# Kernel tuning notes

Hardware: AMD Instinct MI355X
Metric: run time of the kernel (lower is better)

The kernel has to match this reference:

```python
import jax, jax.numpy as jnp
import numpy as np

N = 16384
E = 262144
IN = 512
H = 64
K = 8


def setup_inputs() -> dict:
    key = jax.random.key(0)
    ks = jax.random.split(key, 16)
    def lin(k, fan_in, fan_out):
        # xavier_uniform
        lim = float(np.sqrt(6.0 / (fan_in + fan_out)))
        return jax.random.uniform(k, (fan_in, fan_out), jnp.float32, -lim, lim)
    inp = {
        'x': jax.random.normal(ks[0], (N, IN), jnp.float32),
        'edge_index': jax.random.randint(ks[1], (2, E), 0, N, jnp.int64) if jax.config.read('jax_enable_x64') else jax.random.randint(ks[1], (2, E), 0, N, jnp.int32),
        'W1': lin(ks[2], IN, H), 'b1': jnp.zeros((H,), jnp.float32),
        'W2': lin(ks[3], H, H), 'b2': jnp.zeros((H,), jnp.float32),
        'W3': lin(ks[4], H, H), 'b3': jnp.zeros((H,), jnp.float32),
        'W4': lin(ks[5], H, H), 'b4': jnp.zeros((H,), jnp.float32),
        'Wg1': lin(ks[6], H, H), 'bg1': jnp.zeros((H,), jnp.float32),
        'Wg2': lin(ks[7], H, H), 'bg2': jnp.zeros((H,), jnp.float32),
    }
    return inp


def reference(x, edge_index, W1, b1, W2, b2, W3, b3, W4, b4, Wg1, bg1, Wg2, bg2):
    n = x.shape[0]
    row, col = edge_index[0], edge_index[1]
    # symmetric-normalized Laplacian action: L v = v - D^-1/2 A D^-1/2 v
    deg = jax.ops.segment_sum(jnp.ones(row.shape[0], x.dtype), row, num_segments=n)
    dinv = jnp.where(deg > 0, jax.lax.rsqrt(jnp.maximum(deg, 1e-30)), 0.0)
    # spectral embedding MLP stack (dropout=0 -> identity)
    h = jnp.maximum(x @ W1 + b1, 0.0) @ W2 + b2
    h = jnp.maximum(h @ W3 + b3, 0.0) @ W4 + b4
    g = jnp.maximum(h @ Wg1 + bg1, 0.0) @ Wg2 + bg2  # [N, H]
    msg = (dinv[row] * dinv[col])[:, None] * g[col]   # [E, H]
    agg = jax.ops.segment_sum(msg, row, num_segments=n)
    filtered = g - agg                                 # L @ gft_x
    sim = filtered @ filtered.T                        # [N, N], dominant cost
    topk_vals, topk_idx = jax.lax.top_k(sim, K)        # [N, K]
    src = jnp.repeat(jnp.arange(n, dtype=topk_idx.dtype), K)
    new_edge_index = jnp.stack([src, topk_idx.reshape(-1)])  # [2, N*K]
    return topk_vals, new_edge_index
```

## Files before the change

kernel.cpp:

```cpp
#include <hip/hip_runtime.h>
#include <hip/hip_bf16.h>

#define N_NODES 16384
#define E_EDGES 262144
#define IN_DIM 512
#define KKEEP 56

#define AGG_SCALE 1099511627776.0
#define AGG_INV   (1.0/1099511627776.0)

typedef __attribute__((ext_vector_type(8))) short bf16x8;
typedef __attribute__((ext_vector_type(4))) float f32x4;

__device__ __forceinline__ int detect64(const void* __restrict__ ei) {
    const unsigned long long v = ((const unsigned long long*)ei)[threadIdx.x & 63];
    return __all(v < 16384ull) ? 1 : 0;
}

__device__ __forceinline__ int edge_at(const void* __restrict__ ei, int is64, int pos) {
    return is64 ? (int)(((const long long*)ei)[pos]) : ((const int*)ei)[pos];
}

__global__ __launch_bounds__(256) void deg_kernel(const void* __restrict__ ei,
                                                  int* __restrict__ deg) {
    const int is64 = detect64(ei);
    int e = blockIdx.x * 256 + threadIdx.x;
    int r = edge_at(ei, is64, e);
    if (r >= 0 && r < N_NODES) atomicAdd(&deg[r], 1);
}

__global__ __launch_bounds__(256) void scan_kernel(const int* __restrict__ deg, int* __restrict__ offs,
                                                   float* __restrict__ dinv) {
    __shared__ int part[257];
    const int t = threadIdx.x;
    const int base = t * 64;
    int s = 0;
    #pragma unroll 4
    for (int i = 0; i < 64; ++i) s += deg[base + i];
    part[t + 1] = s;
    if (t == 0) part[0] = 0;
    __syncthreads();
    if (t == 0) {
        int acc = 0;
        for (int i = 1; i <= 256; ++i) { acc += part[i]; part[i] = acc; }
    }
    __syncthreads();
    int run = part[t];
    for (int i = 0; i < 64; ++i) {
        const int d = deg[base + i];
        offs[base + i] = run; run += d;
        dinv[base + i] = (d > 0) ? __fdiv_rn(1.0f, __fsqrt_rn((float)d)) : 0.0f;
    }
    if (t == 255) offs[N_NODES] = run;
}

__global__ __launch_bounds__(256) void scatter_kernel(
    const void* __restrict__ ei,
    const int* __restrict__ offs, int* __restrict__ cursor, int* __restrict__ ecol_s)
{
    const int is64 = detect64(ei);
    int e = blockIdx.x * 256 + threadIdx.x;
    int r  = edge_at(ei, is64, e);
    if (r < 0 || r >= N_NODES) return;
    int cc = edge_at(ei, is64, E_EDGES + e);
    int pos = atomicAdd(&cursor[r], 1);
    ecol_s[offs[r] + pos] = (cc >= 0 && cc < N_NODES) ? cc : -1;
}

__device__ __forceinline__ void dense_layer32(float (*hsw)[64], int c,
                                              const float* __restrict__ WP,
                                              const float* __restrict__ BP,
                                              bool relu, bool last,
                                              float* __restrict__ gout, int n0)
{
    float s0 = 0.0f, s1 = 0.0f, s2 = 0.0f, s3 = 0.0f;
    #pragma unroll 4
    for (int k = 0; k < 64; k += 4) {
        const float4 h0 = *(const float4*)&hsw[0][k];
        const float4 h1 = *(const float4*)&hsw[1][k];
        const float4 h2 = *(const float4*)&hsw[2][k];
        const float4 h3 = *(const float4*)&hsw[3][k];
        const float w0 = WP[k * 64 + c];
        const float w1 = WP[(k + 1) * 64 + c];
        const float w2 = WP[(k + 2) * 64 + c];
        const float w3 = WP[(k + 3) * 64 + c];
        s0 = fmaf(h0.x, w0, s0); s0 = fmaf(h0.y, w1, s0); s0 = fmaf(h0.z, w2, s0); s0 = fmaf(h0.w, w3, s0);
        s1 = fmaf(h1.x, w0, s1); s1 = fmaf(h1.y, w1, s1); s1 = fmaf(h1.z, w2, s1); s1 = fmaf(h1.w, w3, s1);
        s2 = fmaf(h2.x, w0, s2); s2 = fmaf(h2.y, w1, s2); s2 = fmaf(h2.z, w2, s2); s2 = fmaf(h2.w, w3, s2);
        s3 = fmaf(h3.x, w0, s3); s3 = fmaf(h3.y, w1, s3); s3 = fmaf(h3.z, w2, s3); s3 = fmaf(h3.w, w3, s3);
    }
    const float bv = BP[c];
    s0 += bv; s1 += bv; s2 += bv; s3 += bv;
    if (relu) { s0 = fmaxf(s0, 0.0f); s1 = fmaxf(s1, 0.0f); s2 = fmaxf(s2, 0.0f); s3 = fmaxf(s3, 0.0f); }
    __syncthreads();
    if (last) {
        gout[(size_t)(n0 + 0) * 64 + c] = s0;
        gout[(size_t)(n0 + 1) * 64 + c] = s1;
        gout[(size_t)(n0 + 2) * 64 + c] = s2;
        gout[(size_t)(n0 + 3) * 64 + c] = s3;
    } else {
        hsw[0][c] = s0; hsw[1][c] = s1; hsw[2][c] = s2; hsw[3][c] = s3;
    }
    __syncthreads();
}

__global__ __launch_bounds__(256) void mlp_kernel(
    const float* __restrict__ x,
    const float* __restrict__ W1, const float* __restrict__ b1,
    const float* __restrict__ W2, const float* __restrict__ b2,
    const float* __restrict__ W3, const float* __restrict__ b3,
    const float* __restrict__ W4, const float* __restrict__ b4,
    const float* __restrict__ Wg1, const float* __restrict__ bg1,
    const float* __restrict__ Wg2, const float* __restrict__ bg2,
    float* __restrict__ g32)
{
    __shared__ float hs[4][4][64];
    const int w = threadIdx.x >> 6;
    const int c = threadIdx.x & 63;
    const int n0 = blockIdx.x * 16 + w * 4;

    float a0 = 0.0f, a1 = 0.0f, a2 = 0.0f, a3 = 0.0f;
    const float* xp = x + (size_t)n0 * IN_DIM;
    #pragma unroll 2
    for (int k = 0; k < IN_DIM; k += 4) {
        const float4 x0 = *(const float4*)(xp + k);
        const float4 x1 = *(const float4*)(xp + IN_DIM + k);
        const float4 x2 = *(const float4*)(xp + 2 * IN_DIM + k);
        const float4 x3 = *(const float4*)(xp + 3 * IN_DIM + k);
        const float w0 = W1[k * 64 + c];
        const float w1 = W1[(k + 1) * 64 + c];
        const float w2 = W1[(k + 2) * 64 + c];
        const float w3 = W1[(k + 3) * 64 + c];
        a0 = fmaf(x0.x, w0, a0); a0 = fmaf(x0.y, w1, a0); a0 = fmaf(x0.z, w2, a0); a0 = fmaf(x0.w, w3, a0);
        a1 = fmaf(x1.x, w0, a1); a1 = fmaf(x1.y, w1, a1); a1 = fmaf(x1.z, w2, a1); a1 = fmaf(x1.w, w3, a1);
        a2 = fmaf(x2.x, w0, a2); a2 = fmaf(x2.y, w1, a2); a2 = fmaf(x2.z, w2, a2); a2 = fmaf(x2.w, w3, a2);
        a3 = fmaf(x3.x, w0, a3); a3 = fmaf(x3.y, w1, a3); a3 = fmaf(x3.z, w2, a3); a3 = fmaf(x3.w, w3, a3);
    }
    const float bv = b1[c];
    hs[w][0][c] = fmaxf(a0 + bv, 0.0f);
    hs[w][1][c] = fmaxf(a1 + bv, 0.0f);
    hs[w][2][c] = fmaxf(a2 + bv, 0.0f);
    hs[w][3][c] = fmaxf(a3 + bv, 0.0f);
    __syncthreads();

    dense_layer32(hs[w], c, W2, b2, false, false, g32, n0);
    dense_layer32(hs[w], c, W3, b3, true,  false, g32, n0);
    dense_layer32(hs[w], c, W4, b4, false, false, g32, n0);
    dense_layer32(hs[w], c, Wg1, bg1, true, false, g32, n0);
    dense_layer32(hs[w], c, Wg2, bg2, false, true, g32, n0);
}

__global__ __launch_bounds__(256) void aggcsr_kernel(
    const int* __restrict__ offs, const int* __restrict__ ecol_s,
    const float* __restrict__ dinv, const float* __restrict__ g32,
    float* __restrict__ F32, short* __restrict__ Fb)
{
    const int r = (blockIdx.x << 2) + (threadIdx.x >> 6);
    const int h = threadIdx.x & 63;
    const float dr = dinv[r];
    const int b = offs[r], e2 = offs[r + 1];
    long long sum = 0;
    #pragma unroll 8
    for (int i = b; i < e2; ++i) {
        const int cc = ecol_s[i];
        if (cc < 0) continue;
        const float m = __fmul_rn(__fmul_rn(dr, dinv[cc]), g32[((size_t)cc << 6) + h]);
        sum += __double2ll_rn((double)m * AGG_SCALE);
    }
    const float a = (float)((double)sum * AGG_INV);
    const int idx = (r << 6) + h;
    const float f = g32[idx] - a;
    F32[idx] = f;
    __hip_bfloat16 hb = __float2bfloat16(f);
    Fb[idx] = *(short*)&hb;
}

__device__ __forceinline__ void ins6(unsigned* k, unsigned x) {
    const unsigned r0 = max(k[0], x);
    k[5] = min(k[4], max(k[5], x));
    k[4] = min(k[3], max(k[4], x));
    k[3] = min(k[2], max(k[3], x));
    k[2] = min(k[1], max(k[2], x));
    k[1] = min(k[0], max(k[1], x));
    k[0] = r0;
}

__global__ __launch_bounds__(256) void screen_kernel(
    const short* __restrict__ Fb, unsigned* __restrict__ cand)
{
    __shared__ short Bt[2][128 * 64];
    const int l = threadIdx.x & 63;
    const int w = threadIdx.x >> 6;
    const int rb = blockIdx.x >> 1;
    const int sp = blockIdx.x & 1;
    const int r0 = rb * 64 + w * 16;
    const int c0 = sp * 8192;

    const short* ap = Fb + ((size_t)(r0 + (l & 15)) << 6) + ((l >> 4) << 3);
    const bf16x8 a0 = *(const bf16x8*)(ap);
    const bf16x8 a1 = *(const bf16x8*)(ap + 32);

    unsigned keys[4][6];
    #pragma unroll
    for (int r = 0; r < 4; ++r)
        #pragma unroll
        for (int t = 0; t < 6; ++t) keys[r][t] = 0u;

    const int scol = threadIdx.x & 127;
    const int jb = (threadIdx.x >> 7) * 4;
    const short* gsrc0 = Fb + ((size_t)(c0 + scol) << 6) + jb * 8;

    bf16x8 st[4];
    #pragma unroll
    for (int j = 0; j < 4; ++j) st[j] = *(const bf16x8*)(gsrc0 + j * 8);
    #pragma unroll
    for (int j = 0; j < 4; ++j)
        *(bf16x8*)(&Bt[0][scol * 64 + (((jb + j) ^ (scol & 7)) << 3)]) = st[j];
    #pragma unroll
    for (int j = 0; j < 4; ++j) st[j] = *(const bf16x8*)(gsrc0 + (1 << 13) + j * 8);
    __syncthreads();

    const unsigned invb = 0x80000000u | (unsigned)(16383 - c0 - (l & 15));
    const int g0 = (l >> 4) ^ (l & 7);
    const int g1 = ((l >> 4) + 4) ^ (l & 7);
    int cur = 0;

    #pragma unroll 1
    for (int t = 0; t < 64; ++t) {
        const short* B = &Bt[cur][0];
        bf16x8 bf[16];
        #pragma unroll
        for (int s = 0; s < 8; ++s) {
            const int C = s * 16 + (l & 15);
            bf[2 * s]     = *(const bf16x8*)(B + C * 64 + (g0 << 3));
            bf[2 * s + 1] = *(const bf16x8*)(B + C * 64 + (g1 << 3));
        }
        if (t + 1 < 64) {
            #pragma unroll
            for (int j = 0; j < 4; ++j)
                *(bf16x8*)(&Bt[cur ^ 1][scol * 64 + (((jb + j) ^ (scol & 7)) << 3)]) = st[j];
        }
        if (t + 2 < 64) {
            const short* gs = gsrc0 + ((size_t)(t + 2) << 13);
            #pragma unroll
            for (int j = 0; j < 4; ++j) st[j] = *(const bf16x8*)(gs + j * 8);
        }
        #pragma unroll
        for (int s = 0; s < 8; ++s) {
            f32x4 acc = {0.0f, 0.0f, 0.0f, 0.0f};
            acc = __builtin_amdgcn_mfma_f32_16x16x32_bf16(a0, bf[2 * s], acc, 0, 0, 0);
            acc = __builtin_amdgcn_mfma_f32_16x16x32_bf16(a1, bf[2 * s + 1], acc, 0, 0, 0);
            const unsigned xv = invb - (unsigned)((t << 7) + (s << 4));
            #pragma unroll
            for (int r = 0; r < 4; ++r) {
                const unsigned key = (__float_as_uint(acc[r]) & 0xFFFFC000u) ^ xv;
                ins6(keys[r], key);
            }
        }
        __syncthreads();
        cur ^= 1;
    }

    #pragma unroll
    for (int r = 0; r < 4; ++r) {
        const int row = r0 + ((l >> 4) << 2) + r;
        unsigned* cp = cand + ((size_t)(sp * N_NODES + row)) * 96 + (l & 15) * 6;
        #pragma unroll
        for (int t = 0; t < 6; ++t) cp[t] = keys[r][t];
    }
}

__global__ __launch_bounds__(512) void refine2_kernel(
    const float* __restrict__ F, const unsigned* __restrict__ cand,
    float* __restrict__ out)
{
    __shared__ unsigned skey[2][192];
    __shared__ int clist[2][64];
    __shared__ float scand[2][KKEEP * 68];
    const int tid = threadIdx.x;
    const int half = tid >> 8;
    const int th = tid & 255;

    const int ksp = (th >= 96) ? 1 : 0;
    const int kslot = th - 96 * ksp;

    unsigned kreg = 0u;
    {
        const int row0 = blockIdx.x * 2 + half;
        if (th < 192) kreg = cand[((size_t)(ksp * N_NODES + row0)) * 96 + kslot];
    }

    #pragma unroll 1
    for (int i = 0; i < 8; ++i) {
        const int row = blockIdx.x * 2 + half + i * 2048;
        if (th < 192) skey[half][th] = kreg;
        __syncthreads();

        if (i + 1 < 8 && th < 192)
            kreg = cand[((size_t)(ksp * N_NODES + (row + 2048))) * 96 + kslot];

        if (th < 64) {
            const unsigned k0 = skey[half][th], k1 = skey[half][th + 64], k2 = skey[half][th + 128];
            unsigned long long lo = 0, hi = 0xFFFFFFFFull;
            while (hi - lo > 1) {
                const unsigned mid = (unsigned)((lo + hi) >> 1);
                const int cnt = __popcll(__ballot(k0 >= mid)) +
                                __popcll(__ballot(k1 >= mid)) +
                                __popcll(__ballot(k2 >= mid));
                if (cnt >= KKEEP) lo = mid; else hi = mid;
            }
            const unsigned thr = (unsigned)lo;
            const unsigned long long m0 = __ballot(k0 >= thr);
            const unsigned long long m1 = __ballot(k1 >= thr);
            const unsigned long long m2 = __ballot(k2 >= thr);
            const unsigned long long ltm = (1ull << th) - 1ull;
            const int b1 = __popcll(m0), b2 = b1 + __popcll(m1);
            if (k0 >= thr) clist[half][__popcll(m0 & ltm)]      = 16383 - (int)(k0 & 0x3FFFu);
            if (k1 >= thr) clist[half][b1 + __popcll(m1 & ltm)] = 16383 - (int)(k1 & 0x3FFFu);
            if (k2 >= thr) clist[half][b2 + __popcll(m2 & ltm)] = 16383 - (int)(k2 & 0x3FFFu);
        }
        __syncthreads();

        if (th < KKEEP * 4) {
            const int g = th >> 2, sub = th & 3;
            const float* src = F + ((size_t)clist[half][g] << 6) + sub * 16;
            float* dst = &scand[half][g * 68 + sub * 16];
            #pragma unroll
            for (int j = 0; j < 4; ++j)
                *(float4*)(dst + 4 * j) = *(const float4*)(src + 4 * j);
        }
        __syncthreads();

        float val = -3.4e38f; int idx = 1 << 30;
        if (th < KKEEP) {
            idx = clist[half][th];
            const float* fp = &scand[half][th * 68];
            const float* frp = F + ((size_t)row << 6);
            float acc = 0.0f;
            #pragma unroll 4
            for (int j = 0; j < 16; ++j) {
                const float4 a = *(const float4*)(frp + 4 * j);
                const float4 b = *(const float4*)(fp + 4 * j);
                acc = fmaf(a.x, b.x, acc);
                acc = fmaf(a.y, b.y, acc);
                acc = fmaf(a.z, b.z, acc);
                acc = fmaf(a.w, b.w, acc);
            }
            val = acc;
        }
        if (th < 64) {
            #pragma unroll 1
            for (int it = 0; it < 8; ++it) {
                float bv = val; int bi = idx;
                #pragma unroll
                for (int off = 32; off > 0; off >>= 1) {
                    const float ov = __shfl_xor(bv, off);
                    const int   oi = __shfl_xor(bi, off);
                    if (ov > bv || (ov == bv && oi < bi)) { bv = ov; bi = oi; }
                }
                if (th == 0) {
                    out[(size_t)row * 8 + it]          = bv;
                    out[131072 + (size_t)row * 8 + it] = (float)row;
                    out[262144 + (size_t)row * 8 + it] = (float)bi;
                }
                if (idx == bi) val = -3.4e38f;
            }
        }
    }
}

__global__ void canary_kernel(float* out, float code) {
    out[0] = code;
}

extern "C" void kernel_launch(void* const* d_in, const int* in_sizes, int n_in,
                              void* d_out, int out_size, void* d_ws, size_t ws_size,
                              hipStream_t stream)
{
    const float* x   = (const float*)d_in[0];
    const void*  ei  = d_in[1];
    const float* W1  = (const float*)d_in[2];  const float* b1  = (const float*)d_in[3];
    const float* W2  = (const float*)d_in[4];  const float* b2  = (const float*)d_in[5];
    const float* W3  = (const float*)d_in[6];  const float* b3  = (const float*)d_in[7];
    const float* W4  = (const float*)d_in[8];  const float* b4  = (const float*)d_in[9];
    const float* Wg1 = (const float*)d_in[10]; const float* bg1 = (const float*)d_in[11];
    const float* Wg2 = (const float*)d_in[12]; const float* bg2 = (const float*)d_in[13];
    float* out = (float*)d_out;

    char* ws = (char*)d_ws;
    float* g32 = (float*)(ws);
    float* F32 = (float*)(ws + ((size_t)4 << 20));
    short* Fb  = (short*)(ws + ((size_t)8 << 20));
    unsigned* cand = (unsigned*)(ws + ((size_t)10 << 20));
    int*   ecol_s = (int*)(ws + ((size_t)10 << 20));
    int*   offs   = (int*)(ws + ((size_t)11 << 20));
    int*   deg    = (int*)(ws + ((size_t)23 << 20));
    int*   cursor = (int*)(ws + ((size_t)23 << 20) + (1u << 16));
    float* dinvf  = (float*)(ws + ((size_t)23 << 20) + (2u << 16));

    const size_t NEEDED = ((size_t)23 << 20) + (3u << 16);
    if (ws_size < NEEDED || n_in < 14) {
        canary_kernel<<<1, 1, 0, stream>>>(out, ws_size < NEEDED ? 5000.0f : 3000.0f);
        return;
    }

    hipMemsetAsync(deg, 0, 2 * N_NODES * sizeof(int), stream);

    deg_kernel<<<E_EDGES / 256, 256, 0, stream>>>(ei, deg);
    scan_kernel<<<1, 256, 0, stream>>>(deg, offs, dinvf);
    scatter_kernel<<<E_EDGES / 256, 256, 0, stream>>>(ei, offs, cursor, ecol_s);
    mlp_kernel<<<N_NODES / 16, 256, 0, stream>>>(x, W1, b1, W2, b2, W3, b3, W4, b4, Wg1, bg1, Wg2, bg2, g32);
    aggcsr_kernel<<<N_NODES / 4, 256, 0, stream>>>(offs, ecol_s, dinvf, g32, F32, Fb);
    screen_kernel<<<512, 256, 0, stream>>>(Fb, cand);
    refine2_kernel<<<1024, 512, 0, stream>>>(F32, cand, out);
}
```

Baseline: 391.4 us.

## Split screen kernel column tiles across two waves per row strip and merge top-k

The screen kernel now launches 512 threads per block. Each 16-row strip is handled by two waves, and each wave processes half of the 128-column tile. This doubles the number of waves available to hide MFMA, LDS and insertion-sort latency, and halves the per-thread staging load. At the end, the per-wave top-6 key lists are merged through shared memory. The merge adds an extra barrier, a shared-memory exchange and more register pressure per block.

```diff
diff --git a/kernel.cpp b/kernel.cpp
--- a/kernel.cpp
+++ b/kernel.cpp
@@ -185,15 +185,18 @@
     k[0] = r0;
 }
 
-__global__ __launch_bounds__(256) void screen_kernel(
+__global__ __launch_bounds__(512) void screen_kernel(
     const short* __restrict__ Fb, unsigned* __restrict__ cand)
 {
     __shared__ short Bt[2][128 * 64];
-    const int l = threadIdx.x & 63;
-    const int w = threadIdx.x >> 6;
+    const int tid = threadIdx.x;
+    const int l = tid & 63;
+    const int w = tid >> 6;
+    const int strip = w >> 1;
+    const int half = w & 1;
     const int rb = blockIdx.x >> 1;
     const int sp = blockIdx.x & 1;
-    const int r0 = rb * 64 + w * 16;
+    const int r0 = rb * 64 + strip * 16;
     const int c0 = sp * 8192;
 
     const short* ap = Fb + ((size_t)(r0 + (l & 15)) << 6) + ((l >> 4) << 3);
@@ -206,51 +209,52 @@
         #pragma unroll
         for (int t = 0; t < 6; ++t) keys[r][t] = 0u;
 
-    const int scol = threadIdx.x & 127;
-    const int jb = (threadIdx.x >> 7) * 4;
-    const short* gsrc0 = Fb + ((size_t)(c0 + scol) << 6) + jb * 8;
-
-    bf16x8 st[4];
+    const int scol = tid & 127;
+    const int j0 = (tid >> 7) * 2;
+    const short* gsrc0 = Fb + ((size_t)(c0 + scol) << 6) + j0 * 8;
+
+    bf16x8 st[2];
     #pragma unroll
-    for (int j = 0; j < 4; ++j) st[j] = *(const bf16x8*)(gsrc0 + j * 8);
+    for (int j = 0; j < 2; ++j) st[j] = *(const bf16x8*)(gsrc0 + j * 8);
     #pragma unroll
-    for (int j = 0; j < 4; ++j)
-        *(bf16x8*)(&Bt[0][scol * 64 + (((jb + j) ^ (scol & 7)) << 3)]) = st[j];
+    for (int j = 0; j < 2; ++j)
+        *(bf16x8*)(&Bt[0][scol * 64 + (((j0 + j) ^ (scol & 7)) << 3)]) = st[j];
     #pragma unroll
-    for (int j = 0; j < 4; ++j) st[j] = *(const bf16x8*)(gsrc0 + (1 << 13) + j * 8);
+    for (int j = 0; j < 2; ++j) st[j] = *(const bf16x8*)(gsrc0 + (1 << 13) + j * 8);
     __syncthreads();
 
     const unsigned invb = 0x80000000u | (unsigned)(16383 - c0 - (l & 15));
     const int g0 = (l >> 4) ^ (l & 7);
     const int g1 = ((l >> 4) + 4) ^ (l & 7);
+    const int sbase = half * 4;
     int cur = 0;
 
     #pragma unroll 1
     for (int t = 0; t < 64; ++t) {
         const short* B = &Bt[cur][0];
-        bf16x8 bf[16];
+        bf16x8 bf[8];
         #pragma unroll
-        for (int s = 0; s < 8; ++s) {
-            const int C = s * 16 + (l & 15);
-            bf[2 * s]     = *(const bf16x8*)(B + C * 64 + (g0 << 3));
-            bf[2 * s + 1] = *(const bf16x8*)(B + C * 64 + (g1 << 3));
+        for (int ss = 0; ss < 4; ++ss) {
+            const int C = (sbase + ss) * 16 + (l & 15);
+            bf[2 * ss]     = *(const bf16x8*)(B + C * 64 + (g0 << 3));
+            bf[2 * ss + 1] = *(const bf16x8*)(B + C * 64 + (g1 << 3));
         }
         if (t + 1 < 64) {
             #pragma unroll
-            for (int j = 0; j < 4; ++j)
-                *(bf16x8*)(&Bt[cur ^ 1][scol * 64 + (((jb + j) ^ (scol & 7)) << 3)]) = st[j];
+            for (int j = 0; j < 2; ++j)
+                *(bf16x8*)(&Bt[cur ^ 1][scol * 64 + (((j0 + j) ^ (scol & 7)) << 3)]) = st[j];
         }
         if (t + 2 < 64) {
             const short* gs = gsrc0 + ((size_t)(t + 2) << 13);
             #pragma unroll
-            for (int j = 0; j < 4; ++j) st[j] = *(const bf16x8*)(gs + j * 8);
+            for (int j = 0; j < 2; ++j) st[j] = *(const bf16x8*)(gs + j * 8);
         }
         #pragma unroll
-        for (int s = 0; s < 8; ++s) {
+        for (int ss = 0; ss < 4; ++ss) {
             f32x4 acc = {0.0f, 0.0f, 0.0f, 0.0f};
-            acc = __builtin_amdgcn_mfma_f32_16x16x32_bf16(a0, bf[2 * s], acc, 0, 0, 0);
-            acc = __builtin_amdgcn_mfma_f32_16x16x32_bf16(a1, bf[2 * s + 1], acc, 0, 0, 0);
-            const unsigned xv = invb - (unsigned)((t << 7) + (s << 4));
+            acc = __builtin_amdgcn_mfma_f32_16x16x32_bf16(a0, bf[2 * ss], acc, 0, 0, 0);
+            acc = __builtin_amdgcn_mfma_f32_16x16x32_bf16(a1, bf[2 * ss + 1], acc, 0, 0, 0);
+            const unsigned xv = invb - (unsigned)((t << 7) + ((sbase + ss) << 4));
             #pragma unroll
             for (int r = 0; r < 4; ++r) {
                 const unsigned key = (__float_as_uint(acc[r]) & 0xFFFFC000u) ^ xv;
@@ -261,12 +265,29 @@
         cur ^= 1;
     }
 
-    #pragma unroll
-    for (int r = 0; r < 4; ++r) {
-        const int row = r0 + ((l >> 4) << 2) + r;
-        unsigned* cp = cand + ((size_t)(sp * N_NODES + row)) * 96 + (l & 15) * 6;
+    __syncthreads();
+    unsigned* mbuf = (unsigned*)&Bt[0][0];
+    if (half == 1) {
         #pragma unroll
-        for (int t = 0; t < 6; ++t) cp[t] = keys[r][t];
+        for (int r = 0; r < 4; ++r)
+            #pragma unroll
+            for (int t = 0; t < 6; ++t)
+                mbuf[(strip * 64 + l) * 24 + r * 6 + t] = keys[r][t];
+    }
+    __syncthreads();
+    if (half == 0) {
+        #pragma unroll
+        for (int r = 0; r < 4; ++r) {
+            unsigned m[6];
+            #pragma unroll
+            for (int t = 0; t < 6; ++t) m[t] = keys[r][t];
+            #pragma unroll
+            for (int t = 0; t < 6; ++t) ins6(m, mbuf[(strip * 64 + l) * 24 + r * 6 + t]);
+            const int row = r0 + ((l >> 4) << 2) + r;
+            unsigned* cp = cand + ((size_t)(sp * N_NODES + row)) * 96 + (l & 15) * 6;
+            #pragma unroll
+            for (int t = 0; t < 6; ++t) cp[t] = m[t];
+        }
     }
 }
 
@@ -411,6 +432,6 @@
     scatter_kernel<<<E_EDGES / 256, 256, 0, stream>>>(ei, offs, cursor, ecol_s);
     mlp_kernel<<<N_NODES / 16, 256, 0, stream>>>(x, W1, b1, W2, b2, W3, b3, W4, b4, Wg1, bg1, Wg2, bg2, g32);
     aggcsr_kernel<<<N_NODES / 4, 256, 0, stream>>>(offs, ecol_s, dinvf, g32, F32, Fb);
-    screen_kernel<<<512, 256, 0, stream>>>(Fb, cand);
+    screen_kernel<<<512, 512, 0, stream>>>(Fb, cand);
     refine2_kernel<<<1024, 512, 0, stream>>>(F32, cand, out);
 }
```

Measured after the change: 396.1 us. No clear change (+1.2%).
